# Kernel tuning notes

Hardware: AMD Instinct MI355X
Metric: run time of the kernel (lower is better)

The kernel has to match this reference:

```python
import jax, jax.numpy as jnp
import numpy as np


def setup_inputs() -> dict:
    key = jax.random.key(0)
    k1, k2, k3, k4 = jax.random.split(key, 4)
    B, D, F = 524288, 64, 32
    stdv = 1.0 / np.sqrt(D)
    x = jax.random.normal(k1, (B, D), dtype=jnp.float32)
    us = jax.random.uniform(k2, (F, D), dtype=jnp.float32, minval=-stdv, maxval=stdv)
    ws = jax.random.uniform(k3, (F, D), dtype=jnp.float32, minval=-stdv, maxval=stdv)
    bs = jax.random.uniform(k4, (F,), dtype=jnp.float32, minval=-0.01, maxval=0.01)
    return {"x": x, "us": us, "ws": ws, "bs": bs}


def _planar_step(carry, params):
    z, sum_log_det = carry
    u, w, b = params  # u,w: [D], b: scalar
    # constrained u for invertibility: u_hat = u + (softplus(wu) - 1 - wu) * w / ||w||
    wu = jnp.dot(u, w)
    u_hat = u + (jax.nn.softplus(wu) - 1.0 - wu) * w / jnp.linalg.norm(w)
    lin = z @ w + b                      # [B]
    h = jnp.tanh(lin)                    # [B]
    z_new = z + u_hat[None, :] * h[:, None]
    h_prime = 1.0 - h * h                # [B]
    # psi @ u_hat = h'(lin) * (w . u_hat)
    log_det = jnp.log(jnp.abs(1.0 + h_prime * jnp.dot(w, u_hat)))
    return (z_new, sum_log_det + log_det), None


def reference(x, us, ws, bs):
    init = (x, jnp.zeros(x.shape[0], dtype=x.dtype))
    (z, sum_log_det), _ = jax.lax.scan(_planar_step, init, (us, ws, bs))
    return z, sum_log_det
```

## Files before the change

kernel.cpp:

```cpp
#include <hip/hip_runtime.h>
#include <math.h>


#define NF_D 64
#define NF_F 32

typedef float f4 __attribute__((ext_vector_type(4)));
typedef float f32x4v __attribute__((ext_vector_type(4)));
typedef unsigned int u32;
typedef u32 u32x4 __attribute__((ext_vector_type(4)));
typedef short bf16x8 __attribute__((ext_vector_type(8)));

#define WS_WF   0
#define WS_UF   2048
#define WS_GT   3072
#define WS_WUH  4096
#define WS_TOT  4128

__device__ __forceinline__ u32 fbits(float x){ union{float f;u32 u;} c; c.f=x; return c.u; }
__device__ __forceinline__ float asf(u32 u){ union{u32 u;float f;} c; c.u=u; return c.f; }
__device__ __forceinline__ u32 bfrnd(float x){ u32 b=fbits(x); return (b + 0x7FFFu + ((b>>16)&1u)) >> 16; }
__device__ __forceinline__ bf16x8 asbf(u32x4 v){ union{u32x4 u; bf16x8 b;} c; c.u=v; return c.b; }

__global__ void nf_precompute(const float* __restrict__ us,
                              const float* __restrict__ ws,
                              u32* __restrict__ wsb) {
  __shared__ float s_u[NF_F][NF_D];
  float* wsf = (float*)wsb;
  int t = threadIdx.x;
  if (t < NF_F) {
    const float* u = us + t * NF_D;
    const float* w = ws + t * NF_D;
    float wu = 0.f, n2 = 0.f;
    for (int d = 0; d < NF_D; ++d) {
      wu = fmaf(u[d], w[d], wu);
      n2 = fmaf(w[d], w[d], n2);
    }
    float sp = fmaxf(wu, 0.f) + log1pf(expf(-fabsf(wu)));
    float coef = (sp - 1.f - wu) / sqrtf(n2);
    for (int d = 0; d < NF_D; ++d)
      s_u[t][d] = fmaf(coef, w[d], u[d]);
    wsf[WS_WUH + t] = fmaf(coef, n2, wu);
  }
  __syncthreads();
  for (int idx = t; idx < 8 * 64; idx += 256) {
    int lin = idx >> 6, l = idx & 63;
    int Mt = lin >> 2, Kt = (lin >> 1) & 1, p = lin & 1;
    int fm = 16 * Mt + (l & 15);
    int kb = 32 * Kt + 8 * (l >> 4);
    for (int i = 0; i < 4; ++i) {
      u32 pr[2];
      for (int e = 0; e < 2; ++e) {
        float w = ws[fm * NF_D + kb + 2 * i + e];
        u32 hb = fbits(w) & 0xFFFF0000u;
        pr[e] = (p == 0) ? (hb >> 16) : (fbits(w - asf(hb)) >> 16);
      }
      wsb[WS_WF + (lin * 64 + l) * 4 + i] = pr[0] | (pr[1] << 16);
    }
  }
  for (int idx = t; idx < 4 * 64; idx += 256) {
    int l = idx & 63;
    int d = 16 * (idx >> 6) + (l & 15);
    int fb = 8 * (l >> 4);
    for (int i = 0; i < 4; ++i) {
      u32 r0 = bfrnd(s_u[fb + 2 * i][d]);
      u32 r1 = bfrnd(s_u[fb + 2 * i + 1][d]);
      wsb[WS_UF + idx * 4 + i] = r0 | (r1 << 16);
    }
  }
  for (int i = t; i < NF_F * NF_F; i += 256) {
    int f = i >> 5, g = i & 31;
    float s = 0.f;
    if (g < f) {
      const float* w = ws + f * NF_D;
      for (int d = 0; d < NF_D; ++d) s = fmaf(s_u[g][d], w[d], s);
    }
    wsf[WS_GT + i] = s;
  }
}

__device__ __forceinline__ float fast_tanh(float x) {
  float e = __builtin_amdgcn_exp2f(x * 2.885390081777927f);
  return 1.f - 2.f * __builtin_amdgcn_rcpf(e + 1.f);
}

#define MFMA __builtin_amdgcn_mfma_f32_16x16x32_bf16

__global__ __launch_bounds__(256) void nf_main(
    const float* __restrict__ x,
    const float* __restrict__ bs,
    const u32* __restrict__ wsb,
    float* __restrict__ out_z,
    float* __restrict__ out_ld,
    int B) {
  __shared__ float S[4][64 * 33];
  __shared__ float Gl[NF_F * NF_F + 2 * NF_F];
  const float* wsf = (const float*)wsb;

  for (int i = threadIdx.x; i < NF_F * NF_F; i += 256)
    Gl[i] = wsf[WS_GT + i];
  if (threadIdx.x < NF_F) {
    Gl[NF_F * NF_F + threadIdx.x] = wsf[WS_WUH + threadIdx.x];
    Gl[NF_F * NF_F + NF_F + threadIdx.x] = bs[threadIdx.x];
  }
  __syncthreads();

  int wave = threadIdx.x >> 6;
  int l = threadIdx.x & 63;
  int ntiles = B / 64;
  int tile = blockIdx.x * 4 + wave;
  if (tile >= ntiles) tile = ntiles - 1;
  float* Sw = S[wave];

  bf16x8 Wf[2][2][2], Uf[4];
  #pragma unroll
  for (int q = 0; q < 8; ++q)
    Wf[q >> 2][(q >> 1) & 1][q & 1] =
        asbf(*(const u32x4*)(wsb + WS_WF + (q * 64 + l) * 4));
  #pragma unroll
  for (int Nt = 0; Nt < 4; ++Nt)
    Uf[Nt] = asbf(*(const u32x4*)(wsb + WS_UF + (Nt * 64 + l) * 4));

  const float* xt = x + (size_t)tile * 64 * NF_D;

  #pragma unroll
  for (int Nt = 0; Nt < 4; ++Nt) {
    bf16x8 Xr[2];
    #pragma unroll
    for (int Kt = 0; Kt < 2; ++Kt) {
      const f4* xp = (const f4*)(xt + ((l & 15) + 16 * Nt) * NF_D +
                                 32 * Kt + 8 * (l >> 4));
      f4 xa = xp[0], xb = xp[1];
      u32x4 pw;
      pw[0] = bfrnd(xa.x) | (bfrnd(xa.y) << 16);
      pw[1] = bfrnd(xa.z) | (bfrnd(xa.w) << 16);
      pw[2] = bfrnd(xb.x) | (bfrnd(xb.y) << 16);
      pw[3] = bfrnd(xb.z) | (bfrnd(xb.w) << 16);
      Xr[Kt] = asbf(pw);
    }
    #pragma unroll
    for (int Mt = 0; Mt < 2; ++Mt) {
      f32x4v a = {0.f, 0.f, 0.f, 0.f};
      #pragma unroll
      for (int Kt = 0; Kt < 2; ++Kt) {
        a = MFMA(Wf[Mt][Kt][0], Xr[Kt], a, 0, 0, 0);
        a = MFMA(Wf[Mt][Kt][1], Xr[Kt], a, 0, 0, 0);
      }
      #pragma unroll
      for (int r = 0; r < 4; ++r)
        Sw[((l & 15) + 16 * Nt) * 33 + 16 * Mt + 4 * (l >> 4) + r] = a[r];
    }
  }

  const float* gt = Gl;
  const float* wuhp = Gl + NF_F * NF_F;
  const float* bsl = Gl + NF_F * NF_F + NF_F;
  f4 hq[8];
  #pragma unroll
  for (int q = 0; q < 8; ++q) hq[q] = (f4)(0.f);
  float ldp = 1.f;
  #pragma unroll
  for (int f = 0; f < NF_F; ++f) {
    const f4* g4 = (const f4*)(gt + f * 32);
    f4 a = (f4)(0.f);
    #pragma unroll
    for (int q = 0; q < (f + 3) / 4; ++q)
      a += g4[q] * hq[q];
    float s = Sw[l * 33 + f] + bsl[f] + ((a.x + a.y) + (a.z + a.w));
    float hf = fast_tanh(s);
    ldp *= fmaf(fmaf(-hf, hf, 1.f), wuhp[f], 1.f);
    hq[f >> 2][f & 3] = hf;
  }
  #pragma unroll
  for (int i = 0; i < 16; ++i) {
    u32 pk = (fbits(hq[i >> 1][(i & 1) * 2]) >> 16) |
             (fbits(hq[i >> 1][(i & 1) * 2 + 1]) & 0xFFFF0000u);
    Sw[i * 64 + l] = asf(pk);
  }

  bf16x8 Hf[4];
  #pragma unroll
  for (int Mt = 0; Mt < 4; ++Mt) {
    u32x4 hw;
    #pragma unroll
    for (int i = 0; i < 4; ++i)
      hw[i] = fbits(Sw[(4 * (l >> 4) + i) * 64 + (l & 15) + 16 * Mt]);
    Hf[Mt] = asbf(hw);
  }

  float* zt = out_z + (size_t)tile * 64 * NF_D;
  #pragma unroll
  for (int Mt = 0; Mt < 4; ++Mt) {
    #pragma unroll
    for (int Nt = 0; Nt < 4; ++Nt) {
      f32x4v zz = {0.f, 0.f, 0.f, 0.f};
      zz = MFMA(Hf[Mt], Uf[Nt], zz, 0, 0, 0);
      #pragma unroll
      for (int r = 0; r < 4; ++r) {
        int brow = 16 * Mt + 4 * (l >> 4) + r;
        int d = (l & 15) + 16 * Nt;
        zt[brow * NF_D + d] = zz[r] + xt[brow * NF_D + d];
      }
    }
  }
  out_ld[(size_t)tile * 64 + l] =
      __builtin_amdgcn_logf(fabsf(ldp)) * 0.6931471805599453f;
}

extern "C" void kernel_launch(void* const* d_in, const int* in_sizes, int n_in,
                              void* d_out, int out_size, void* d_ws, size_t ws_size,
                              hipStream_t stream) {
  const float* x    = (const float*)d_in[0];
  const float* us   = (const float*)d_in[1];
  const float* ws_p = (const float*)d_in[2];
  const float* bs   = (const float*)d_in[3];
  const int B = in_sizes[0] / NF_D;

  u32* wsbuf = (u32*)d_ws;
  float* out = (float*)d_out;

  nf_precompute<<<1, 256, 0, stream>>>(us, ws_p, wsbuf);
  const int ntiles = B / 64;
  const int grid = (ntiles + 3) / 4;
  nf_main<<<grid, 256, 0, stream>>>(x, bs, wsbuf, out,
                                    out + (size_t)B * NF_D, B);
}
```

Measured before the change: 77.74 us.

## Process two tiles per wave and prefetch second tile's input during first

Each wave now handles two 64-row tiles. It loads the second tile's x into registers before running the sequential tanh recurrence for the first tile, so global load latency is hidden behind compute. The grid is halved accordingly. This raises register pressure (16 extra float4 registers), which may lower occupancy, and it drops the tail bounds clamp, so it assumes B is a multiple of 512.

```diff
diff --git a/kernel.cpp b/kernel.cpp
--- a/kernel.cpp
+++ b/kernel.cpp
@@ -107,9 +107,8 @@
 
   int wave = threadIdx.x >> 6;
   int l = threadIdx.x & 63;
-  int ntiles = B / 64;
-  int tile = blockIdx.x * 4 + wave;
-  if (tile >= ntiles) tile = ntiles - 1;
+  int tile0 = (blockIdx.x * 4 + wave) * 2;
+  int tile1 = tile0 + 1;
   float* Sw = S[wave];
 
   bf16x8 Wf[2][2][2], Uf[4];
@@ -121,22 +120,29 @@
   for (int Nt = 0; Nt < 4; ++Nt)
     Uf[Nt] = asbf(*(const u32x4*)(wsb + WS_UF + (Nt * 64 + l) * 4));
 
-  const float* xt = x + (size_t)tile * 64 * NF_D;
+  const float* xt0 = x + (size_t)tile0 * 64 * NF_D;
+  const float* xt1 = x + (size_t)tile1 * 64 * NF_D;
+
+  const float* gt = Gl;
+  const float* wuhp = Gl + NF_F * NF_F;
+  const float* bsl = Gl + NF_F * NF_F + NF_F;
+
+  #define CVT8(xa, xb, dst) { u32x4 pw_;                        \
+      pw_[0] = bfrnd((xa).x) | (bfrnd((xa).y) << 16);           \
+      pw_[1] = bfrnd((xa).z) | (bfrnd((xa).w) << 16);           \
+      pw_[2] = bfrnd((xb).x) | (bfrnd((xb).y) << 16);           \
+      pw_[3] = bfrnd((xb).z) | (bfrnd((xb).w) << 16);           \
+      dst = asbf(pw_); }
 
   #pragma unroll
   for (int Nt = 0; Nt < 4; ++Nt) {
     bf16x8 Xr[2];
     #pragma unroll
     for (int Kt = 0; Kt < 2; ++Kt) {
-      const f4* xp = (const f4*)(xt + ((l & 15) + 16 * Nt) * NF_D +
+      const f4* xp = (const f4*)(xt0 + ((l & 15) + 16 * Nt) * NF_D +
                                  32 * Kt + 8 * (l >> 4));
       f4 xa = xp[0], xb = xp[1];
-      u32x4 pw;
-      pw[0] = bfrnd(xa.x) | (bfrnd(xa.y) << 16);
-      pw[1] = bfrnd(xa.z) | (bfrnd(xa.w) << 16);
-      pw[2] = bfrnd(xb.x) | (bfrnd(xb.y) << 16);
-      pw[3] = bfrnd(xb.z) | (bfrnd(xb.w) << 16);
-      Xr[Kt] = asbf(pw);
+      CVT8(xa, xb, Xr[Kt]);
     }
     #pragma unroll
     for (int Mt = 0; Mt < 2; ++Mt) {
@@ -152,59 +158,97 @@
     }
   }
 
-  const float* gt = Gl;
-  const float* wuhp = Gl + NF_F * NF_F;
-  const float* bsl = Gl + NF_F * NF_F + NF_F;
-  f4 hq[8];
-  #pragma unroll
-  for (int q = 0; q < 8; ++q) hq[q] = (f4)(0.f);
-  float ldp = 1.f;
-  #pragma unroll
-  for (int f = 0; f < NF_F; ++f) {
-    const f4* g4 = (const f4*)(gt + f * 32);
-    f4 a = (f4)(0.f);
-    #pragma unroll
-    for (int q = 0; q < (f + 3) / 4; ++q)
-      a += g4[q] * hq[q];
-    float s = Sw[l * 33 + f] + bsl[f] + ((a.x + a.y) + (a.z + a.w));
-    float hf = fast_tanh(s);
-    ldp *= fmaf(fmaf(-hf, hf, 1.f), wuhp[f], 1.f);
-    hq[f >> 2][f & 3] = hf;
-  }
-  #pragma unroll
-  for (int i = 0; i < 16; ++i) {
-    u32 pk = (fbits(hq[i >> 1][(i & 1) * 2]) >> 16) |
-             (fbits(hq[i >> 1][(i & 1) * 2 + 1]) & 0xFFFF0000u);
-    Sw[i * 64 + l] = asf(pk);
-  }
-
-  bf16x8 Hf[4];
-  #pragma unroll
-  for (int Mt = 0; Mt < 4; ++Mt) {
-    u32x4 hw;
-    #pragma unroll
-    for (int i = 0; i < 4; ++i)
-      hw[i] = fbits(Sw[(4 * (l >> 4) + i) * 64 + (l & 15) + 16 * Mt]);
-    Hf[Mt] = asbf(hw);
-  }
-
-  float* zt = out_z + (size_t)tile * 64 * NF_D;
-  #pragma unroll
-  for (int Mt = 0; Mt < 4; ++Mt) {
-    #pragma unroll
-    for (int Nt = 0; Nt < 4; ++Nt) {
-      f32x4v zz = {0.f, 0.f, 0.f, 0.f};
-      zz = MFMA(Hf[Mt], Uf[Nt], zz, 0, 0, 0);
-      #pragma unroll
-      for (int r = 0; r < 4; ++r) {
-        int brow = 16 * Mt + 4 * (l >> 4) + r;
-        int d = (l & 15) + 16 * Nt;
-        zt[brow * NF_D + d] = zz[r] + xt[brow * NF_D + d];
-      }
-    }
-  }
-  out_ld[(size_t)tile * 64 + l] =
-      __builtin_amdgcn_logf(fabsf(ldp)) * 0.6931471805599453f;
+  f4 x1r[16];
+  #pragma unroll
+  for (int Nt = 0; Nt < 4; ++Nt)
+    #pragma unroll
+    for (int Kt = 0; Kt < 2; ++Kt) {
+      const f4* xp = (const f4*)(xt1 + ((l & 15) + 16 * Nt) * NF_D +
+                                 32 * Kt + 8 * (l >> 4));
+      x1r[(Nt * 2 + Kt) * 2]     = xp[0];
+      x1r[(Nt * 2 + Kt) * 2 + 1] = xp[1];
+    }
+  __builtin_amdgcn_sched_barrier(0);
+
+  float ldres[2];
+  #pragma unroll
+  for (int half = 0; half < 2; ++half) {
+    f4 hq[8];
+    #pragma unroll
+    for (int q = 0; q < 8; ++q) hq[q] = (f4)(0.f);
+    float ldp = 1.f;
+    #pragma unroll
+    for (int f = 0; f < NF_F; ++f) {
+      const f4* g4 = (const f4*)(gt + f * 32);
+      f4 a = (f4)(0.f);
+      #pragma unroll
+      for (int q = 0; q < (f + 3) / 4; ++q)
+        a += g4[q] * hq[q];
+      float s = Sw[l * 33 + f] + bsl[f] + ((a.x + a.y) + (a.z + a.w));
+      float hf = fast_tanh(s);
+      ldp *= fmaf(fmaf(-hf, hf, 1.f), wuhp[f], 1.f);
+      hq[f >> 2][f & 3] = hf;
+    }
+    ldres[half] = ldp;
+    #pragma unroll
+    for (int i = 0; i < 16; ++i) {
+      u32 pk = (fbits(hq[i >> 1][(i & 1) * 2]) >> 16) |
+               (fbits(hq[i >> 1][(i & 1) * 2 + 1]) & 0xFFFF0000u);
+      Sw[i * 64 + l] = asf(pk);
+    }
+
+    bf16x8 Hf[4];
+    #pragma unroll
+    for (int Mt = 0; Mt < 4; ++Mt) {
+      u32x4 hw;
+      #pragma unroll
+      for (int i = 0; i < 4; ++i)
+        hw[i] = fbits(Sw[(4 * (l >> 4) + i) * 64 + (l & 15) + 16 * Mt]);
+      Hf[Mt] = asbf(hw);
+    }
+    const float* xt = half ? xt1 : xt0;
+    int tile = half ? tile1 : tile0;
+    float* zt = out_z + (size_t)tile * 64 * NF_D;
+    #pragma unroll
+    for (int Mt = 0; Mt < 4; ++Mt) {
+      #pragma unroll
+      for (int Nt = 0; Nt < 4; ++Nt) {
+        f32x4v zz = {0.f, 0.f, 0.f, 0.f};
+        zz = MFMA(Hf[Mt], Uf[Nt], zz, 0, 0, 0);
+        #pragma unroll
+        for (int r = 0; r < 4; ++r) {
+          int brow = 16 * Mt + 4 * (l >> 4) + r;
+          int d = (l & 15) + 16 * Nt;
+          zt[brow * NF_D + d] = zz[r] + xt[brow * NF_D + d];
+        }
+      }
+    }
+    out_ld[(size_t)tile * 64 + l] =
+        __builtin_amdgcn_logf(fabsf(ldres[half])) * 0.6931471805599453f;
+
+    if (half == 0) {
+      #pragma unroll
+      for (int Nt = 0; Nt < 4; ++Nt) {
+        bf16x8 Xr[2];
+        #pragma unroll
+        for (int Kt = 0; Kt < 2; ++Kt)
+          CVT8(x1r[(Nt * 2 + Kt) * 2], x1r[(Nt * 2 + Kt) * 2 + 1], Xr[Kt]);
+        #pragma unroll
+        for (int Mt = 0; Mt < 2; ++Mt) {
+          f32x4v a = {0.f, 0.f, 0.f, 0.f};
+          #pragma unroll
+          for (int Kt = 0; Kt < 2; ++Kt) {
+            a = MFMA(Wf[Mt][Kt][0], Xr[Kt], a, 0, 0, 0);
+            a = MFMA(Wf[Mt][Kt][1], Xr[Kt], a, 0, 0, 0);
+          }
+          #pragma unroll
+          for (int r = 0; r < 4; ++r)
+            Sw[((l & 15) + 16 * Nt) * 33 + 16 * Mt + 4 * (l >> 4) + r] = a[r];
+        }
+      }
+    }
+  }
+  #undef CVT8
 }
 
 extern "C" void kernel_launch(void* const* d_in, const int* in_sizes, int n_in,
@@ -221,7 +265,7 @@
 
   nf_precompute<<<1, 256, 0, stream>>>(us, ws_p, wsbuf);
   const int ntiles = B / 64;
-  const int grid = (ntiles + 3) / 4;
+  const int grid = ntiles / 8;
   nf_main<<<grid, 256, 0, stream>>>(x, bs, wsbuf, out,
                                     out + (size_t)B * NF_D, B);
 }
```

Result: slower. 101.7 us (+30.8%).
